# Kernel tuning notes

Hardware: AMD Instinct MI355X
Metric: run time of the kernel (lower is better)

Reference implementation:

```python
import jax, jax.numpy as jnp
import numpy as np

N_HEADS = 8
D_HEAD = 64  # n_embd=512 / n_heads=8


def setup_inputs() -> dict:
    key = jax.random.key(0)
    ks = jax.random.split(key, 5)
    B, T, C = 2, 4096, 512
    x = jax.random.normal(ks[0], (B, T, C), dtype=jnp.float32)
    s = 1.0 / np.sqrt(C)
    Wq = jax.random.normal(ks[1], (C, C), dtype=jnp.float32) * s
    Wk = jax.random.normal(ks[2], (C, C), dtype=jnp.float32) * s
    Wv = jax.random.normal(ks[3], (C, C), dtype=jnp.float32) * s
    Wout = jax.random.normal(ks[4], (C, C), dtype=jnp.float32) * s
    return {"x": x, "Wq": Wq, "Wk": Wk, "Wv": Wv, "Wout": Wout}


def reference(x, Wq, Wk, Wv, Wout):
    # x: [B,T,C]; nn.Linear(y) = y @ W.T, here weights stored as [C,C] used directly
    B, T, C = x.shape
    H, D = N_HEADS, D_HEAD
    q = (x @ Wq.T).reshape(B, T, H, D).transpose(0, 2, 1, 3)  # [B,H,T,D]
    k = (x @ Wk.T).reshape(B, T, H, D).transpose(0, 2, 1, 3)
    v = (x @ Wv.T).reshape(B, T, H, D).transpose(0, 2, 1, 3)
    att = jnp.einsum('bhqd,bhkd->bhqk', q, k) / jnp.sqrt(jnp.float32(D))  # [B,H,T,T]
    causal = jnp.tril(jnp.ones((T, T), dtype=bool))
    att = jnp.where(causal, att, -jnp.inf)
    att = jax.nn.softmax(att, axis=-1)
    # dropout is identity in eval mode (p=0)
    y = jnp.einsum('bhqk,bhkd->bhqd', att, v)  # [B,H,T,D]
    y = y.transpose(0, 2, 1, 3).reshape(B, T, C)
    return y @ Wout.T
```

## Files before the change

### kernel.cpp

```cpp
#include <hip/hip_runtime.h>
#include <hip/hip_bf16.h>
#include <math.h>
#include <stdint.h>

using bf16 = __hip_bfloat16;
typedef __attribute__((ext_vector_type(8))) short short8;
typedef __attribute__((ext_vector_type(4))) short short4v;
typedef __attribute__((ext_vector_type(4))) float float4v;

#define MFMA16(a, b, c) __builtin_amdgcn_mfma_f32_16x16x32_bf16(a, b, c, 0, 0, 0)

__device__ __forceinline__ short bfbits(float f) {
  bf16 h = (bf16)f;
  return *(short*)&h;
}

__device__ __forceinline__ short8 ld_cvt8(const float* p) {
  union { float4v v[2]; float f[8]; } u;
  u.v[0] = *(const float4v*)p;
  u.v[1] = *(const float4v*)(p + 4);
  short8 r;
#pragma unroll
  for (int j = 0; j < 8; j++) r[j] = bfbits(u.f[j]);
  return r;
}

__global__ __launch_bounds__(256) void conv_all(
    const float* __restrict__ x, const float* __restrict__ w0,
    const float* __restrict__ w1, const float* __restrict__ w2,
    const float* __restrict__ w3, bf16* __restrict__ cx,
    bf16* __restrict__ cw) {
  size_t gid = ((size_t)blockIdx.x * 256 + threadIdx.x) * 8;
  const float* src;
  bf16* dst;
  size_t off;
  if (gid < 4194304) {
    src = x; dst = cx; off = gid;
  } else {
    size_t r = gid - 4194304;
    int wi = (int)(r >> 18);
    src = wi == 0 ? w0 : wi == 1 ? w1 : wi == 2 ? w2 : w3;
    dst = cw + ((size_t)wi << 18);
    off = r & 262143;
  }
  *(short8*)(dst + off) = ld_cvt8(src + off);
}

template <int MODE, int MT>
__device__ __forceinline__ void gemm_body(bf16* As, bf16* Bs,
                                          const bf16* __restrict__ A,
                                          const bf16* __restrict__ W,
                                          void* __restrict__ outp,
                                          float oscale) {
  constexpr int STR = 40;
  constexpr int MI = MT / 32;
  const int bm = blockIdx.x * MT, bn = blockIdx.y * 128;
  const int tid = threadIdx.x;
  const int lane = tid & 63;
  const int wave = tid >> 6;
  const int lr = lane & 15, quad = lane >> 4;
  const int wm = (wave & 1) * (MT / 2), wn = (wave >> 1) * 64;

  const int lrow = tid >> 2;
  const int lcol = (tid & 3) * 8;
  const bf16* a0 = A + (size_t)(bm + lrow) * 512 + lcol;
  const bf16* a1 = a0 + (size_t)64 * 512;
  const bf16* b0 = W + (size_t)(bn + lrow) * 512 + lcol;
  const bf16* b1 = b0 + (size_t)64 * 512;
  bf16* as0 = &As[lrow * STR + lcol];
  bf16* as1 = &As[(lrow + 64) * STR + lcol];
  bf16* bs0 = &Bs[lrow * STR + lcol];
  bf16* bs1 = &Bs[(lrow + 64) * STR + lcol];

  short8 ra0, ra1, rb0, rb1;
  ra0 = *(const short8*)a0;
  if (MT == 128) ra1 = *(const short8*)a1;
  rb0 = *(const short8*)b0;
  rb1 = *(const short8*)b1;

  float4v acc[MI][4] = {};

  for (int k0 = 0; k0 < 512; k0 += 32) {
    __syncthreads();
    *(short8*)as0 = ra0;
    if (MT == 128) *(short8*)as1 = ra1;
    *(short8*)bs0 = rb0;
    *(short8*)bs1 = rb1;
    __syncthreads();
    if (k0 + 32 < 512) {
      ra0 = *(const short8*)(a0 + k0 + 32);
      if (MT == 128) ra1 = *(const short8*)(a1 + k0 + 32);
      rb0 = *(const short8*)(b0 + k0 + 32);
      rb1 = *(const short8*)(b1 + k0 + 32);
    }
    short8 af[MI], bfv[4];
#pragma unroll
    for (int i = 0; i < MI; i++)
      af[i] = *(const short8*)&As[(wm + i * 16 + lr) * STR + quad * 8];
#pragma unroll
    for (int i = 0; i < 4; i++)
      bfv[i] = *(const short8*)&Bs[(wn + i * 16 + lr) * STR + quad * 8];
#pragma unroll
    for (int mi = 0; mi < MI; mi++)
#pragma unroll
      for (int ni = 0; ni < 4; ni++)
        acc[mi][ni] = MFMA16(af[mi], bfv[ni], acc[mi][ni]);
  }

  const int row0 = bm + wm + quad * 4;
  const int col0 = bn + wn + lr;
#pragma unroll
  for (int mi = 0; mi < MI; mi++) {
#pragma unroll
    for (int ni = 0; ni < 4; ni++) {
      const int col = col0 + ni * 16;
      if (MODE == 1) {
        float* out = (float*)outp;
#pragma unroll
        for (int i = 0; i < 4; i++) {
          int m = row0 + mi * 16 + i;
          out[(size_t)m * 512 + col] = acc[mi][ni][i];
        }
      } else if (MODE == 0) {
        bf16* out = (bf16*)outp;
        const int hh = col >> 6, d = col & 63;
#pragma unroll
        for (int i = 0; i < 4; i++) {
          int m = row0 + mi * 16 + i;
          int bb = m >> 12, t = m & 4095;
          out[(((size_t)(bb * 8 + hh) * 4096 + t) << 6) + d] =
              (bf16)(acc[mi][ni][i] * oscale);
        }
      } else {
        bf16* out = (bf16*)outp;
        const int hh = col >> 6, d = col & 63;
        int m0 = row0 + mi * 16;
        int bb = m0 >> 12, t0 = m0 & 4095;
        short4v pk;
#pragma unroll
        for (int i = 0; i < 4; i++) pk[i] = bfbits(acc[mi][ni][i]);
        *(short4v*)&out[(((size_t)(bb * 8 + hh) * 64 + d) << 12) + t0] = pk;
      }
    }
  }
}

#define QSCALE 0.18033688f

__global__ __launch_bounds__(256) void qkv_kernel(
    const bf16* __restrict__ cx, const bf16* __restrict__ cW,
    bf16* q, bf16* k, bf16* vt) {
  __shared__ __align__(16) bf16 As[128 * 40];
  __shared__ __align__(16) bf16 Bs[128 * 40];
  if (blockIdx.z == 0)      gemm_body<0, 128>(As, Bs, cx, cW, q, QSCALE);
  else if (blockIdx.z == 1) gemm_body<0, 128>(As, Bs, cx, cW + 262144, k, 1.0f);
  else                      gemm_body<2, 128>(As, Bs, cx, cW + 2 * 262144, vt, 1.0f);
}

__global__ __launch_bounds__(256) void proj_kernel(
    const bf16* __restrict__ y, const bf16* __restrict__ cWout,
    float* __restrict__ out) {
  __shared__ __align__(16) bf16 As[64 * 40];
  __shared__ __align__(16) bf16 Bs[128 * 40];
  gemm_body<1, 64>(As, Bs, y, cWout, out, 1.0f);
}

__device__ __forceinline__ int lsw(int row, int col) {
  return (row << 6) + (col ^ ((row & 7) << 3));
}

template <bool DIAG>
__device__ __forceinline__ void soft_pv(const float4v (&S)[4],
                                        const short8 (&vf)[4][2], bf16* Pw,
                                        int rowb, int lr, int quad,
                                        float* l_i, float4v* O) {
#pragma unroll
  for (int nc = 0; nc < 4; nc++) {
#pragma unroll
    for (int i = 0; i < 4; i++) {
      float p = exp2f(S[nc][i]);
      if (DIAG) {
        int col = nc * 16 + lr;
        p = (col > rowb + i) ? 0.f : p;
      }
      l_i[i] += p;
      Pw[lsw(quad * 4 + i, nc * 16 + lr)] = (bf16)p;
    }
  }
  __threadfence_block();
  short8 pf0 = *(const short8*)&Pw[lsw(lr, quad * 8)];
  short8 pf1 = *(const short8*)&Pw[lsw(lr, 32 + quad * 8)];
#pragma unroll
  for (int nc = 0; nc < 4; nc++) {
    O[nc] = MFMA16(pf0, vf[nc][0], O[nc]);
    O[nc] = MFMA16(pf1, vf[nc][1], O[nc]);
  }
}

__global__ __launch_bounds__(256, 4) void attn_kernel(const bf16* __restrict__ Qg,
                                                      const bf16* __restrict__ Kg,
                                                      const bf16* __restrict__ Vtg,
                                                      bf16* __restrict__ Y) {
  constexpr int T = 4096;
  __shared__ __align__(16) bf16 Ks[2][64 * 64];
  __shared__ __align__(16) bf16 Vts[2][64 * 64];
  __shared__ __align__(16) bf16 Ps[4][16 * 64];

  const int bx = blockIdx.x;
  const int qt = 63 - (bx >> 4);
  const int hb = bx & 15;
  const int h = hb >> 1, b = hb & 1;
  const size_t ho = ((size_t)(b * 8 + h)) * T * 64;
  const bf16* Qh = Qg + ho;
  const bf16* Kh = Kg + ho;
  const bf16* Vth = Vtg + ho;

  const int tid = threadIdx.x;
  const int wave = tid >> 6, lane = tid & 63;
  const int lr = lane & 15, quad = lane >> 4;
  const int rowb = wave * 16 + quad * 4;

  const int sr = tid >> 3;
  const int sc = (tid & 7) * 8;
  const bf16* ksrc0 = Kh + (size_t)sr * 64 + sc;
  const bf16* ksrc1 = ksrc0 + 32 * 64;
  const bf16* vsrc0 = Vth + (size_t)sr * T + sc;
  const bf16* vsrc1 = vsrc0 + (size_t)32 * T;
  const int d0 = lsw(sr, sc);
  const int d1 = lsw(sr + 32, sc);

  short8 rk0 = *(const short8*)ksrc0;
  short8 rk1 = *(const short8*)ksrc1;
  short8 rv0 = *(const short8*)vsrc0;
  short8 rv1 = *(const short8*)vsrc1;

  short8 qf0, qf1;
  for (int s = tid; s < 512; s += 256) {
    int r = s >> 3, c = (s & 7) * 8;
    *(short8*)&Ks[1][lsw(r, c)] =
        *(const short8*)&Qh[(size_t)(qt * 64 + r) * 64 + c];
  }
  __syncthreads();
  qf0 = *(const short8*)&Ks[1][lsw(wave * 16 + lr, quad * 8)];
  qf1 = *(const short8*)&Ks[1][lsw(wave * 16 + lr, 32 + quad * 8)];
  *(short8*)&Ks[0][d0] = rk0;
  *(short8*)&Ks[0][d1] = rk1;
  *(short8*)&Vts[0][d0] = rv0;
  *(short8*)&Vts[0][d1] = rv1;
  __syncthreads();

  float l_i[4] = {};
  float4v O[4] = {};
  bf16* Pw = &Ps[wave][0];

  for (int kt = 0; kt <= qt; kt++) {
    const int cur = kt & 1, nxt = cur ^ 1;
    const bool pf = kt < qt;
    if (pf) {
      const size_t ko = (size_t)(kt + 1) * 4096;
      const size_t vo = (size_t)(kt + 1) * 64;
      rk0 = *(const short8*)(ksrc0 + ko);
      rk1 = *(const short8*)(ksrc1 + ko);
      rv0 = *(const short8*)(vsrc0 + vo);
      rv1 = *(const short8*)(vsrc1 + vo);
    }

    const bf16* Kc = Ks[cur];
    const bf16* Vc = Vts[cur];

    short8 kf[4][2];
#pragma unroll
    for (int nc = 0; nc < 4; nc++) {
      kf[nc][0] = *(const short8*)&Kc[lsw(nc * 16 + lr, quad * 8)];
      kf[nc][1] = *(const short8*)&Kc[lsw(nc * 16 + lr, 32 + quad * 8)];
    }

    float4v S[4] = {};
#pragma unroll
    for (int nc = 0; nc < 4; nc++) {
      S[nc] = MFMA16(qf0, kf[nc][0], S[nc]);
      S[nc] = MFMA16(qf1, kf[nc][1], S[nc]);
    }

    short8 vf[4][2];
#pragma unroll
    for (int nc = 0; nc < 4; nc++) {
      vf[nc][0] = *(const short8*)&Vc[lsw(nc * 16 + lr, quad * 8)];
      vf[nc][1] = *(const short8*)&Vc[lsw(nc * 16 + lr, 32 + quad * 8)];
    }

    if (kt == qt) soft_pv<true>(S, vf, Pw, rowb, lr, quad, l_i, O);
    else          soft_pv<false>(S, vf, Pw, rowb, lr, quad, l_i, O);

    if (pf) {
      *(short8*)&Ks[nxt][d0] = rk0;
      *(short8*)&Ks[nxt][d1] = rk1;
      *(short8*)&Vts[nxt][d0] = rv0;
      *(short8*)&Vts[nxt][d1] = rv1;
    }
    __syncthreads();
  }

#pragma unroll
  for (int off = 1; off < 16; off <<= 1)
#pragma unroll
    for (int i = 0; i < 4; i++) l_i[i] += __shfl_xor(l_i[i], off, 64);
#pragma unroll
  for (int i = 0; i < 4; i++) l_i[i] = 1.f / l_i[i];

  const size_t yb = ((size_t)b * T + qt * 64 + wave * 16 + quad * 4) * 512 + h * 64;
#pragma unroll
  for (int nc = 0; nc < 4; nc++)
#pragma unroll
    for (int i = 0; i < 4; i++)
      Y[yb + (size_t)i * 512 + nc * 16 + lr] = (bf16)(O[nc][i] * l_i[i]);
}

extern "C" void kernel_launch(void* const* d_in, const int* in_sizes, int n_in,
                              void* d_out, int out_size, void* d_ws, size_t ws_size,
                              hipStream_t stream) {
  (void)out_size; (void)ws_size;
  const int NX = 8192 * 512;
  int xi = 0;
  for (int i = 0; i < n_in; i++)
    if (in_sizes[i] == NX) { xi = i; break; }
  const float* x = (const float*)d_in[xi];
  const float* wsrc[4];
  int wn = 0;
  for (int i = 0; i < n_in && wn < 4; i++)
    if (i != xi) wsrc[wn++] = (const float*)d_in[i];

  bf16* ws = (bf16*)d_ws;
  const size_t HE = (size_t)NX;
  bf16* q  = ws;
  bf16* k  = q + HE;
  bf16* yx = k + HE;
  bf16* cw = yx + HE;
  bf16* vt = (bf16*)d_out;
  float* out = (float*)d_out;

  conv_all<<<2560, 256, 0, stream>>>(x, wsrc[0], wsrc[1], wsrc[2], wsrc[3],
                                     yx, cw);
  qkv_kernel<<<dim3(64, 4, 3), 256, 0, stream>>>(yx, cw, q, k, vt);
  attn_kernel<<<1024, 256, 0, stream>>>(q, k, vt, yx);
  proj_kernel<<<dim3(128, 4), 256, 0, stream>>>(yx, cw + 3 * 262144, out);
}
```

Before: 189.7 us.

## Compute S transposed to keep P in registers and rebalance causal tile order

Swaps the MFMA operand order so each lane holds scores for one query row across key columns. The softmax probabilities can then be packed straight into the A-operand registers for the PV MFMA, which removes the per-wave shared-memory P buffer, its fence and its reloads. V fragments are gathered with 4-element loads to match the permuted key ordering. The diagonal tile is peeled out of the loop, row sums now need fewer shuffles, and block-to-query-tile mapping is interleaved so long and short causal tiles mix across the grid; the added cost is a little register shuffling and narrower LDS reads for V.

```diff
diff --git a/kernel.cpp b/kernel.cpp
--- a/kernel.cpp
+++ b/kernel.cpp
@@ -170,30 +170,54 @@
 }
 
 template <bool DIAG>
-__device__ __forceinline__ void soft_pv(const float4v (&S)[4],
-                                        const short8 (&vf)[4][2], bf16* Pw,
-                                        int rowb, int lr, int quad,
-                                        float* l_i, float4v* O) {
+__device__ __forceinline__ void attn_step(const bf16* __restrict__ Kc,
+                                          const bf16* __restrict__ Vc,
+                                          short8 qf0, short8 qf1,
+                                          int wave, int lr, int quad,
+                                          float& l_i, float4v* O) {
+  float4v S[4] = {};
 #pragma unroll
   for (int nc = 0; nc < 4; nc++) {
+    short8 kf0 = *(const short8*)&Kc[lsw(nc * 16 + lr, quad * 8)];
+    short8 kf1 = *(const short8*)&Kc[lsw(nc * 16 + lr, 32 + quad * 8)];
+    S[nc] = MFMA16(kf0, qf0, S[nc]);
+    S[nc] = MFMA16(kf1, qf1, S[nc]);
+  }
+
+  short8 pf0, pf1;
+#pragma unroll
+  for (int nc = 0; nc < 4; nc++) {
 #pragma unroll
     for (int i = 0; i < 4; i++) {
-      float p = exp2f(S[nc][i]);
+      float pv = exp2f(S[nc][i]);
       if (DIAG) {
-        int col = nc * 16 + lr;
-        p = (col > rowb + i) ? 0.f : p;
+        int kl = nc * 16 + quad * 4 + i;
+        pv = (kl > wave * 16 + lr) ? 0.f : pv;
       }
-      l_i[i] += p;
-      Pw[lsw(quad * 4 + i, nc * 16 + lr)] = (bf16)p;
-    }
-  }
-  __threadfence_block();
-  short8 pf0 = *(const short8*)&Pw[lsw(lr, quad * 8)];
-  short8 pf1 = *(const short8*)&Pw[lsw(lr, 32 + quad * 8)];
+      l_i += pv;
+      short bb = bfbits(pv);
+      if (nc == 0)      pf0[i] = bb;
+      else if (nc == 1) pf0[4 + i] = bb;
+      else if (nc == 2) pf1[i] = bb;
+      else              pf1[4 + i] = bb;
+    }
+  }
+
 #pragma unroll
   for (int nc = 0; nc < 4; nc++) {
-    O[nc] = MFMA16(pf0, vf[nc][0], O[nc]);
-    O[nc] = MFMA16(pf1, vf[nc][1], O[nc]);
+    const int row = nc * 16 + lr;
+    short4v va0 = *(const short4v*)&Vc[lsw(row, 4 * quad)];
+    short4v va1 = *(const short4v*)&Vc[lsw(row, 16 + 4 * quad)];
+    short4v vb0 = *(const short4v*)&Vc[lsw(row, 32 + 4 * quad)];
+    short4v vb1 = *(const short4v*)&Vc[lsw(row, 48 + 4 * quad)];
+    short8 vfa, vfb;
+#pragma unroll
+    for (int j = 0; j < 4; j++) {
+      vfa[j] = va0[j]; vfa[4 + j] = va1[j];
+      vfb[j] = vb0[j]; vfb[4 + j] = vb1[j];
+    }
+    O[nc] = MFMA16(pf0, vfa, O[nc]);
+    O[nc] = MFMA16(pf1, vfb, O[nc]);
   }
 }
 
@@ -204,11 +228,11 @@
   constexpr int T = 4096;
   __shared__ __align__(16) bf16 Ks[2][64 * 64];
   __shared__ __align__(16) bf16 Vts[2][64 * 64];
-  __shared__ __align__(16) bf16 Ps[4][16 * 64];
 
   const int bx = blockIdx.x;
-  const int qt = 63 - (bx >> 4);
-  const int hb = bx & 15;
+  const int g = bx >> 8, r = bx & 255;
+  const int a = r >> 4, hb = r & 15;
+  const int qt = (g == 0) ? a : (g == 1) ? 16 + a : (g == 2) ? 63 - a : 47 - a;
   const int h = hb >> 1, b = hb & 1;
   const size_t ho = ((size_t)(b * 8 + h)) * T * 64;
   const bf16* Qh = Qg + ho;
@@ -218,7 +242,6 @@
   const int tid = threadIdx.x;
   const int wave = tid >> 6, lane = tid & 63;
   const int lr = lane & 15, quad = lane >> 4;
-  const int rowb = wave * 16 + quad * 4;
 
   const int sr = tid >> 3;
   const int sc = (tid & 7) * 8;
@@ -236,9 +259,9 @@
 
   short8 qf0, qf1;
   for (int s = tid; s < 512; s += 256) {
-    int r = s >> 3, c = (s & 7) * 8;
-    *(short8*)&Ks[1][lsw(r, c)] =
-        *(const short8*)&Qh[(size_t)(qt * 64 + r) * 64 + c];
+    int rr = s >> 3, c = (s & 7) * 8;
+    *(short8*)&Ks[1][lsw(rr, c)] =
+        *(const short8*)&Qh[(size_t)(qt * 64 + rr) * 64 + c];
   }
   __syncthreads();
   qf0 = *(const short8*)&Ks[1][lsw(wave * 16 + lr, quad * 8)];
@@ -249,14 +272,12 @@
   *(short8*)&Vts[0][d1] = rv1;
   __syncthreads();
 
-  float l_i[4] = {};
+  float l_i = 0.f;
   float4v O[4] = {};
-  bf16* Pw = &Ps[wave][0];
-
-  for (int kt = 0; kt <= qt; kt++) {
+
+  for (int kt = 0; kt < qt; kt++) {
     const int cur = kt & 1, nxt = cur ^ 1;
-    const bool pf = kt < qt;
-    if (pf) {
+    {
       const size_t ko = (size_t)(kt + 1) * 4096;
       const size_t vo = (size_t)(kt + 1) * 64;
       rk0 = *(const short8*)(ksrc0 + ko);
@@ -265,55 +286,29 @@
       rv1 = *(const short8*)(vsrc1 + vo);
     }
 
-    const bf16* Kc = Ks[cur];
-    const bf16* Vc = Vts[cur];
-
-    short8 kf[4][2];
-#pragma unroll
-    for (int nc = 0; nc < 4; nc++) {
-      kf[nc][0] = *(const short8*)&Kc[lsw(nc * 16 + lr, quad * 8)];
-      kf[nc][1] = *(const short8*)&Kc[lsw(nc * 16 + lr, 32 + quad * 8)];
-    }
-
-    float4v S[4] = {};
-#pragma unroll
-    for (int nc = 0; nc < 4; nc++) {
-      S[nc] = MFMA16(qf0, kf[nc][0], S[nc]);
-      S[nc] = MFMA16(qf1, kf[nc][1], S[nc]);
-    }
-
-    short8 vf[4][2];
-#pragma unroll
-    for (int nc = 0; nc < 4; nc++) {
-      vf[nc][0] = *(const short8*)&Vc[lsw(nc * 16 + lr, quad * 8)];
-      vf[nc][1] = *(const short8*)&Vc[lsw(nc * 16 + lr, 32 + quad * 8)];
-    }
-
-    if (kt == qt) soft_pv<true>(S, vf, Pw, rowb, lr, quad, l_i, O);
-    else          soft_pv<false>(S, vf, Pw, rowb, lr, quad, l_i, O);
-
-    if (pf) {
-      *(short8*)&Ks[nxt][d0] = rk0;
-      *(short8*)&Ks[nxt][d1] = rk1;
-      *(short8*)&Vts[nxt][d0] = rv0;
-      *(short8*)&Vts[nxt][d1] = rv1;
-    }
+    attn_step<false>(Ks[cur], Vts[cur], qf0, qf1, wave, lr, quad, l_i, O);
+
+    *(short8*)&Ks[nxt][d0] = rk0;
+    *(short8*)&Ks[nxt][d1] = rk1;
+    *(short8*)&Vts[nxt][d0] = rv0;
+    *(short8*)&Vts[nxt][d1] = rv1;
     __syncthreads();
   }
-
-#pragma unroll
-  for (int off = 1; off < 16; off <<= 1)
-#pragma unroll
-    for (int i = 0; i < 4; i++) l_i[i] += __shfl_xor(l_i[i], off, 64);
-#pragma unroll
-  for (int i = 0; i < 4; i++) l_i[i] = 1.f / l_i[i];
+  attn_step<true>(Ks[qt & 1], Vts[qt & 1], qf0, qf1, wave, lr, quad, l_i, O);
+
+  l_i += __shfl_xor(l_i, 16, 64);
+  l_i += __shfl_xor(l_i, 32, 64);
+  const float linv = 1.f / l_i;
+  float lrow[4];
+#pragma unroll
+  for (int i = 0; i < 4; i++) lrow[i] = __shfl(linv, quad * 4 + i, 64);
 
   const size_t yb = ((size_t)b * T + qt * 64 + wave * 16 + quad * 4) * 512 + h * 64;
 #pragma unroll
   for (int nc = 0; nc < 4; nc++)
 #pragma unroll
     for (int i = 0; i < 4; i++)
-      Y[yb + (size_t)i * 512 + nc * 16 + lr] = (bf16)(O[nc][i] * l_i[i]);
+      Y[yb + (size_t)i * 512 + nc * 16 + lr] = (bf16)(O[nc][i] * lrow[i]);
 }
 
 extern "C" void kernel_launch(void* const* d_in, const int* in_sizes, int n_in,
```

Result: no change. 188.1 us (-0.9%).
